# Kernel optimization log

Hardware: AMD Instinct MI355X
Metric: run time of the kernel (lower is better)

Reference implementation:

```python
import jax, jax.numpy as jnp
import numpy as np

B, T, C = 2, 4096, 768
H = 12
HD = C // H  # 64


def setup_inputs() -> dict:
    key = jax.random.key(0)
    k1, k2, k3 = jax.random.split(key, 3)
    scale = 0.02
    x = jax.random.normal(k1, (B, T, C), dtype=jnp.float32)
    w_attn = jax.random.normal(k2, (C, 3 * C), dtype=jnp.float32) * scale
    b_attn = jnp.zeros((3 * C,), dtype=jnp.float32)
    w_proj = jax.random.normal(k3, (C, C), dtype=jnp.float32) * scale
    b_proj = jnp.zeros((C,), dtype=jnp.float32)
    return {"x": x, "w_attn": w_attn, "b_attn": b_attn,
            "w_proj": w_proj, "b_proj": b_proj}


def reference(x, w_attn, b_attn, w_proj, b_proj):
    b, t, c = x.shape
    # QKV projection: (B,T,3C)
    qkv = x @ w_attn + b_attn
    q, k, v = jnp.split(qkv, 3, axis=2)
    # (B,H,T,HD)
    q = q.reshape(b, t, H, HD).transpose(0, 2, 1, 3)
    k = k.reshape(b, t, H, HD).transpose(0, 2, 1, 3)
    v = v.reshape(b, t, H, HD).transpose(0, 2, 1, 3)
    # scores: (B,H,T,T)
    scores = jnp.einsum('bhqd,bhkd->bhqk', q, k) / jnp.sqrt(jnp.float32(HD))
    causal = jnp.tril(jnp.ones((t, t), dtype=bool))
    scores = jnp.where(causal[None, None, :, :], scores, -jnp.inf)
    att = jax.nn.softmax(scores, axis=-1)
    # attn_dropout p=0 -> identity
    y = jnp.einsum('bhqk,bhkd->bhqd', att, v)
    y = y.transpose(0, 2, 1, 3).reshape(b, t, c)
    # output projection (resid_dropout p=0 -> identity)
    return y @ w_proj + b_proj
```

## Files before the change

kernel.cpp:

```cpp
#include <hip/hip_runtime.h>


typedef unsigned short u16;
typedef unsigned int u32;
using bf16x8 = __attribute__((ext_vector_type(8))) short;
using f32x4  = __attribute__((ext_vector_type(4))) float;

__device__ __forceinline__ float bf2f(u16 u) {
  return __uint_as_float(((u32)u) << 16);
}
__device__ __forceinline__ u16 f2bf(float f) {
  u32 u = __float_as_uint(f);
  u += 0x7fffu + ((u >> 16) & 1u);
  return (u16)(u >> 16);
}
__device__ __forceinline__ u32 cvtpk(float lo, float hi) {
  u32 r;
  asm("v_cvt_pk_bf16_f32 %0, %1, %2" : "=v"(r) : "v"(lo), "v"(hi));
  return r;
}
__device__ __forceinline__ void gload_lds16(const u16* g, u16* l) {
  __builtin_amdgcn_global_load_lds(
      (const __attribute__((address_space(1))) unsigned int*)g,
      (__attribute__((address_space(3))) unsigned int*)l, 16, 0, 0);
}

__global__ void fill_sentinel_f32(float* __restrict__ out, int n, float v) {
  const int i0 = blockIdx.x * blockDim.x + threadIdx.x;
  const int stride = gridDim.x * blockDim.x;
  for (int i = i0; i < n; i += stride) out[i] = v;
}

__global__ void convert_f32_bf16(const float* __restrict__ src, u16* __restrict__ dst,
                                 int n) {
  const int i0 = blockIdx.x * blockDim.x + threadIdx.x;
  const int stride = gridDim.x * blockDim.x;
  for (int i = i0; i < n; i += stride) dst[i] = f2bf(src[i]);
}

__global__ void transpose_f32_bf16(const float* __restrict__ in, u16* __restrict__ out,
                                   int R, int C) {
  __shared__ u16 tile[32][33];
  const int c0 = blockIdx.x * 32, r0 = blockIdx.y * 32;
  const int tx = threadIdx.x & 31, ty = threadIdx.x >> 5;
#pragma unroll
  for (int i = 0; i < 32; i += 8)
    tile[ty + i][tx] = f2bf(in[(size_t)(r0 + ty + i) * C + c0 + tx]);
  __syncthreads();
#pragma unroll
  for (int i = 0; i < 32; i += 8)
    out[(size_t)(c0 + ty + i) * R + r0 + tx] = tile[tx][ty + i];
}

#define QSCALE 0.18033688011112f

template <int MODE>
__global__ __launch_bounds__(256, 3)
void gemm128(const u16* __restrict__ A, const u16* __restrict__ Bt,
             const u16* __restrict__ bias, void* __restrict__ O0v,
             u16* __restrict__ O1, u16* __restrict__ O2, int Kd) {
  __shared__ __align__(16) u16 As[128 * 64];
  __shared__ __align__(16) u16 Bs[128 * 64];
  const int tid = threadIdx.x;
  const int lane = tid & 63, wave = tid >> 6;
  const int wm = wave >> 1, wn = wave & 1;
  const int l16 = lane & 15, quad = lane >> 4;

  const u16* Ag0 = A + (size_t)blockIdx.x * 128 * Kd +
                   (size_t)(tid >> 3) * Kd + (tid & 7) * 8;
  const u16* Bg0 = Bt + (size_t)blockIdx.y * 128 * Kd +
                   (size_t)(tid >> 3) * Kd + (tid & 7) * 8;
  const int ldsb = wave * 512;

  f32x4 acc[4][4] = {};
  for (int kt = 0; kt < Kd; kt += 64) {
#pragma unroll
    for (int i = 0; i < 4; ++i) {
      gload_lds16(Ag0 + (size_t)i * 32 * Kd + kt, &As[i * 2048 + ldsb]);
      gload_lds16(Bg0 + (size_t)i * 32 * Kd + kt, &Bs[i * 2048 + ldsb]);
    }
    __syncthreads();
#pragma unroll
    for (int s = 0; s < 2; ++s) {
      bf16x8 af[4], bfr[4];
#pragma unroll
      for (int i = 0; i < 4; ++i) {
        const int m = wm * 64 + i * 16 + l16;
        af[i] = *(const bf16x8*)&As[m * 64 + (s * 4 + quad) * 8];
        const int n = wn * 64 + i * 16 + l16;
        bfr[i] = *(const bf16x8*)&Bs[n * 64 + (s * 4 + quad) * 8];
      }
#pragma unroll
      for (int i = 0; i < 4; ++i)
#pragma unroll
        for (int j = 0; j < 4; ++j)
          acc[i][j] = __builtin_amdgcn_mfma_f32_16x16x32_bf16(af[i], bfr[j],
                                                              acc[i][j], 0, 0, 0);
    }
    __syncthreads();
  }

#pragma unroll
  for (int i = 0; i < 4; ++i) {
    const int mbase = blockIdx.x * 128 + wm * 64 + i * 16 + quad * 4;
#pragma unroll
    for (int j = 0; j < 4; ++j) {
      const int nb = blockIdx.y * 128 + wn * 64 + j * 16;
      const int n = nb + l16;
      const float bv = bf2f(bias[n]);
      if (MODE == 0) {
        const int which = nb / 768;
        const int b = mbase >> 12, t = mbase & 4095;
        const int c = n - which * 768;
        const int h = c >> 6, d = c & 63;
        const size_t bh = (size_t)b * 12 + h;
        if (which == 0) {
#pragma unroll
          for (int r = 0; r < 4; ++r)
            ((u16*)O0v)[((bh * 4096 + t + r) << 6) + d] =
                f2bf((acc[i][j][r] + bv) * QSCALE);
        } else if (which == 1) {
#pragma unroll
          for (int r = 0; r < 4; ++r)
            O1[((bh * 4096 + t + r) << 6) + d] = f2bf(acc[i][j][r] + bv);
        } else {
          ushort4 pk;
          pk.x = f2bf(acc[i][j][0] + bv);
          pk.y = f2bf(acc[i][j][1] + bv);
          pk.z = f2bf(acc[i][j][2] + bv);
          pk.w = f2bf(acc[i][j][3] + bv);
          *(ushort4*)&O2[((bh << 6) + (size_t)d) * 4096 + t] = pk;
        }
      } else {
#pragma unroll
        for (int r = 0; r < 4; ++r)
          ((float*)O0v)[(size_t)(mbase + r) * 768 + n] = acc[i][j][r] + bv;
      }
    }
  }
}

__global__ __launch_bounds__(256, 3)
void attn_chunk(const u16* __restrict__ Q, const u16* __restrict__ K,
                const u16* __restrict__ Vt, u16* __restrict__ Y,
                u16* __restrict__ part_o, float* __restrict__ part_l) {
  const int idx = blockIdx.x;
  const int bh = idx % 24;
  const int cid = 79 - (idx / 24);
  int qt = 0, base = 0, nc = 1;
  for (int q = 0; q < 32; ++q) {
    const int c = (q >> 3) + 1;
    if (cid < base + c) { qt = q; nc = c; break; }
    base += c;
  }
  const int j = cid - base;
  const int Nt = 2 * qt + 2;
  const int kbeg = j * 16;
  const int kend = (kbeg + 16 < Nt) ? kbeg + 16 : Nt;
  const int q0 = qt * 128;
  const int b = bh / 12, h = bh % 12;
  const size_t ho = (size_t)bh * 4096 * 64;
  const u16* Qg = Q + ho + (size_t)q0 * 64;
  const u16* Kg = K + ho;
  const u16* Vg = Vt + ho;

  __shared__ __align__(16) u16 Ks[3][64 * 64];
  __shared__ __align__(16) u16 Vs[3][64 * 64];

  const int tid = threadIdx.x;
  const int lane = tid & 63, wave = tid >> 6;
  const int l16 = lane & 15, quad = lane >> 4;
  const int sw8 = (l16 & 7) * 8;

  const int rl = tid >> 3, m7 = tid & 7;
  const int cs = (m7 ^ (rl & 7)) * 8;
  const u16* kg0 = Kg + (size_t)rl * 64 + cs;
  const u16* vg0 = Vg + (size_t)rl * 4096 + cs;
  const int wb = wave * 512;

  bf16x8 qf[2][2];
#pragma unroll
  for (int rt = 0; rt < 2; ++rt)
#pragma unroll
    for (int s = 0; s < 2; ++s)
      qf[rt][s] = *(const bf16x8*)&Qg[(wave * 32 + rt * 16 + l16) * 64 + s * 32 + quad * 8];

  bf16x8 ones;
#pragma unroll
  for (int e = 0; e < 8; ++e) ones[e] = (short)0x3F80;

  f32x4 lacc[2] = {};
  f32x4 o[2][4] = {};

  auto stage = [&](int bf, int kt2) {
    const size_t ko = (size_t)kt2 * 4096;
    const int to = kt2 * 64;
    gload_lds16(kg0 + ko,               &Ks[bf][wb]);
    gload_lds16(kg0 + ko + 2048,        &Ks[bf][2048 + wb]);
    gload_lds16(vg0 + to,               &Vs[bf][wb]);
    gload_lds16(vg0 + to + 32 * 4096,   &Vs[bf][2048 + wb]);
  };

  const int ntt = kend - kbeg;
  stage(0, kbeg);
  if (ntt > 1) {
    stage(1, kbeg + 1);
    asm volatile("s_waitcnt vmcnt(4)" ::: "memory");
  } else {
    asm volatile("s_waitcnt vmcnt(0)" ::: "memory");
  }
  __builtin_amdgcn_sched_barrier(0);
  __builtin_amdgcn_s_barrier();
  int cur = 0;

  for (int kt2 = kbeg; kt2 < kend; ++kt2) {
    const int t0 = kt2 * 64;
    const bool pf = (kt2 + 2 < kend);
    if (pf) {
      int nb = cur + 2; if (nb >= 3) nb -= 3;
      stage(nb, kt2 + 2);
    }
    __builtin_amdgcn_sched_barrier(0);

    f32x4 sc[4][2] = {};
#pragma unroll
    for (int s = 0; s < 2; ++s) {
      bf16x8 kf[4];
#pragma unroll
      for (int nt = 0; nt < 4; ++nt)
        kf[nt] = *(const bf16x8*)&Ks[cur][(nt * 16 + l16) * 64 +
                                          ((s * 32 + quad * 8) ^ sw8)];
      __builtin_amdgcn_s_setprio(1);
#pragma unroll
      for (int nt = 0; nt < 4; ++nt)
#pragma unroll
        for (int rt = 0; rt < 2; ++rt)
          sc[nt][rt] = __builtin_amdgcn_mfma_f32_16x16x32_bf16(kf[nt], qf[rt][s],
                                                               sc[nt][rt], 0, 0, 0);
      __builtin_amdgcn_s_setprio(0);
    }

    u32 pw[4][2][2];
#pragma unroll
    for (int rt = 0; rt < 2; ++rt) {
      const int rowb = q0 + wave * 32 + rt * 16;
      if (t0 + 63 <= rowb) {
#pragma unroll
        for (int nt = 0; nt < 4; ++nt) {
          f32x4 p;
#pragma unroll
          for (int r = 0; r < 4; ++r)
            p[r] = __builtin_amdgcn_exp2f(sc[nt][rt][r]);
          pw[nt][rt][0] = cvtpk(p[0], p[1]);
          pw[nt][rt][1] = cvtpk(p[2], p[3]);
        }
      } else {
        const int qrow = rowb + l16;
#pragma unroll
        for (int nt = 0; nt < 4; ++nt) {
          f32x4 p;
#pragma unroll
          for (int r = 0; r < 4; ++r) {
            float pv = __builtin_amdgcn_exp2f(sc[nt][rt][r]);
            if (t0 + nt * 16 + quad * 4 + r > qrow) pv = 0.f;
            p[r] = pv;
          }
          pw[nt][rt][0] = cvtpk(p[0], p[1]);
          pw[nt][rt][1] = cvtpk(p[2], p[3]);
        }
      }
    }

#pragma unroll
    for (int s2 = 0; s2 < 2; ++s2) {
      bf16x8 vf[4];
#pragma unroll
      for (int dt = 0; dt < 4; ++dt) {
        const int vbase = (dt * 16 + l16) * 64;
        const int a1 = vbase + ((s2 * 32 + quad * 4) ^ sw8);
        union { uint2 hv[2]; bf16x8 v; } uv;
        uv.hv[0] = *(const uint2*)&Vs[cur][a1];
        uv.hv[1] = *(const uint2*)&Vs[cur][a1 ^ 16];
        vf[dt] = uv.v;
      }
#pragma unroll
      for (int rt = 0; rt < 2; ++rt) {
        union { u32 w[4]; bf16x8 v; } up;
        up.w[0] = pw[2 * s2][rt][0];
        up.w[1] = pw[2 * s2][rt][1];
        up.w[2] = pw[2 * s2 + 1][rt][0];
        up.w[3] = pw[2 * s2 + 1][rt][1];
        __builtin_amdgcn_s_setprio(1);
#pragma unroll
        for (int dt = 0; dt < 4; ++dt)
          o[rt][dt] = __builtin_amdgcn_mfma_f32_16x16x32_bf16(up.v, vf[dt],
                                                              o[rt][dt], 0, 0, 0);
        lacc[rt] = __builtin_amdgcn_mfma_f32_16x16x32_bf16(up.v, ones,
                                                           lacc[rt], 0, 0, 0);
        __builtin_amdgcn_s_setprio(0);
      }
    }

    if (kt2 + 1 < kend) {
      if (pf) asm volatile("s_waitcnt vmcnt(4)" ::: "memory");
      else    asm volatile("s_waitcnt vmcnt(0)" ::: "memory");
      __builtin_amdgcn_sched_barrier(0);
      __builtin_amdgcn_s_barrier();
      if (++cur == 3) cur = 0;
    }
  }

  if (nc == 1) {
#pragma unroll
    for (int rt = 0; rt < 2; ++rt)
#pragma unroll
      for (int r = 0; r < 4; ++r) {
        const float inv = 1.f / lacc[rt][r];
        const int t = q0 + wave * 32 + rt * 16 + quad * 4 + r;
#pragma unroll
        for (int dt = 0; dt < 4; ++dt)
          Y[((size_t)b * 4096 + t) * 768 + h * 64 + dt * 16 + l16] =
              f2bf(o[rt][dt][r] * inv);
      }
  } else {
    const int pslot = bh * 72 + (cid - 8);
    u16* po = part_o + (size_t)pslot * 8192;
    float* pl = part_l + pslot * 128;
#pragma unroll
    for (int rt = 0; rt < 2; ++rt)
#pragma unroll
      for (int r = 0; r < 4; ++r) {
        const int row = wave * 32 + rt * 16 + quad * 4 + r;
#pragma unroll
        for (int dt = 0; dt < 4; ++dt)
          po[row * 64 + dt * 16 + l16] = f2bf(o[rt][dt][r]);
        if (l16 == 0) pl[row] = lacc[rt][r];
      }
  }
}

__global__ __launch_bounds__(256, 8)
void attn_combine(const u16* __restrict__ part_o, const float* __restrict__ part_l,
                  u16* __restrict__ Y) {
  const int bh = blockIdx.x, qt = 8 + blockIdx.y;
  const int g = qt >> 3, i = qt & 7;
  const int nc = g + 1;
  const int base = 4 * g * (g + 1) + i * (g + 1);
  const int slot0 = bh * 72 + base - 8;
  const int b = bh / 12, h = bh % 12;
  const int q0 = qt * 128;
  for (int e = threadIdx.x; e < 8192; e += 256) {
    const int row = e >> 6, d = e & 63;
    float Os = 0.f, ls = 0.f;
    for (int c = 0; c < nc; ++c) {
      Os += bf2f(part_o[(size_t)(slot0 + c) * 8192 + e]);
      ls += part_l[(slot0 + c) * 128 + row];
    }
    Y[((size_t)b * 4096 + q0 + row) * 768 + h * 64 + d] = f2bf(Os / ls);
  }
}

extern "C" void kernel_launch(void* const* d_in, const int* in_sizes, int n_in,
                              void* d_out, int out_size, void* d_ws, size_t ws_size,
                              hipStream_t stream) {
  (void)in_sizes; (void)n_in;
  const float* x      = (const float*)d_in[0];
  const float* w_attn = (const float*)d_in[1];
  const float* b_attn = (const float*)d_in[2];
  const float* w_proj = (const float*)d_in[3];
  const float* b_proj = (const float*)d_in[4];
  float* out = (float*)d_out;

  char* ws = (char*)d_ws;
  size_t off = 0;
  auto alloc = [&](size_t bytes) -> void* {
    void* p = ws + off;
    off += (bytes + 255) & ~(size_t)255;
    return p;
  };
  u16* xb  = (u16*)alloc((size_t)8192 * 768 * 2);
  u16* WtA = (u16*)alloc((size_t)2304 * 768 * 2);
  u16* WtP = (u16*)alloc((size_t)768 * 768 * 2);
  u16* ba  = (u16*)alloc(2304 * 2);
  u16* bp  = (u16*)alloc(768 * 2);
  u16* Q   = (u16*)alloc((size_t)6291456 * 2);
  u16* Kp  = (u16*)alloc((size_t)6291456 * 2);
  u16* Vt  = (u16*)alloc((size_t)6291456 * 2);
  u16* Y   = (u16*)alloc((size_t)6291456 * 2);
  u16* part_o  = (u16*)alloc((size_t)24 * 72 * 8192 * 2);
  float* part_l = (float*)alloc((size_t)24 * 72 * 128 * 4);

  if (ws_size < off) {
    fill_sentinel_f32<<<256, 256, 0, stream>>>(out, out_size,
                                               100.0f + (float)(ws_size >> 20));
    return;
  }

  convert_f32_bf16<<<2048, 256, 0, stream>>>(x, xb, 8192 * 768);
  convert_f32_bf16<<<16, 256, 0, stream>>>(b_attn, ba, 2304);
  convert_f32_bf16<<<8, 256, 0, stream>>>(b_proj, bp, 768);
  transpose_f32_bf16<<<dim3(72, 24), 256, 0, stream>>>(w_attn, WtA, 768, 2304);
  transpose_f32_bf16<<<dim3(24, 24), 256, 0, stream>>>(w_proj, WtP, 768, 768);

  gemm128<0><<<dim3(64, 18), 256, 0, stream>>>(xb, WtA, ba, Q, Kp, Vt, 768);
  attn_chunk<<<1920, 256, 0, stream>>>(Q, Kp, Vt, Y, part_o, part_l);
  attn_combine<<<dim3(24, 24), 256, 0, stream>>>(part_o, part_l, Y);
  gemm128<1><<<dim3(64, 6), 256, 0, stream>>>(Y, WtP, bp, out, nullptr, nullptr, 768);
}
```

Measured before the change: 273.1 us.

## Fuse prep kernels and load V directly from global into registers

Result: slower. 573.6 us (+110.0%).

```diff
diff --git a/kernel.cpp b/kernel.cpp
--- a/kernel.cpp
+++ b/kernel.cpp
@@ -31,25 +31,44 @@
   for (int i = i0; i < n; i += stride) out[i] = v;
 }
 
-__global__ void convert_f32_bf16(const float* __restrict__ src, u16* __restrict__ dst,
-                                 int n) {
-  const int i0 = blockIdx.x * blockDim.x + threadIdx.x;
-  const int stride = gridDim.x * blockDim.x;
-  for (int i = i0; i < n; i += stride) dst[i] = f2bf(src[i]);
-}
-
-__global__ void transpose_f32_bf16(const float* __restrict__ in, u16* __restrict__ out,
-                                   int R, int C) {
+__global__ __launch_bounds__(256)
+void prep(const float* __restrict__ x, const float* __restrict__ w_attn,
+          const float* __restrict__ b_attn, const float* __restrict__ w_proj,
+          const float* __restrict__ b_proj, u16* __restrict__ xb,
+          u16* __restrict__ WtA, u16* __restrict__ WtP,
+          u16* __restrict__ ba, u16* __restrict__ bp) {
   __shared__ u16 tile[32][33];
-  const int c0 = blockIdx.x * 32, r0 = blockIdx.y * 32;
-  const int tx = threadIdx.x & 31, ty = threadIdx.x >> 5;
-#pragma unroll
-  for (int i = 0; i < 32; i += 8)
-    tile[ty + i][tx] = f2bf(in[(size_t)(r0 + ty + i) * C + c0 + tx]);
-  __syncthreads();
-#pragma unroll
-  for (int i = 0; i < 32; i += 8)
-    out[(size_t)(c0 + ty + i) * R + r0 + tx] = tile[tx][ty + i];
+  const int bid = blockIdx.x, tid = threadIdx.x;
+  if (bid < 2304) {
+    const float* in; u16* out; int R, C, bx, by;
+    if (bid < 1728) { in = w_attn; out = WtA; R = 768; C = 2304;
+                      bx = bid % 72; by = bid / 72; }
+    else            { in = w_proj; out = WtP; R = 768; C = 768;
+                      bx = (bid - 1728) % 24; by = (bid - 1728) / 24; }
+    const int c0 = bx * 32, r0 = by * 32;
+    const int tx = tid & 31, ty = tid >> 5;
+#pragma unroll
+    for (int i = 0; i < 32; i += 8)
+      tile[ty + i][tx] = f2bf(in[(size_t)(r0 + ty + i) * C + c0 + tx]);
+    __syncthreads();
+#pragma unroll
+    for (int i = 0; i < 32; i += 8)
+      out[(size_t)(c0 + ty + i) * R + r0 + tx] = tile[tx][ty + i];
+  } else if (bid < 3328) {
+    const int n4 = 8192 * 768 / 4;
+    const int i0 = (bid - 2304) * 256 + tid, stride = 1024 * 256;
+    const float4* src = (const float4*)x;
+    ushort4* dst = (ushort4*)xb;
+    for (int i = i0; i < n4; i += stride) {
+      const float4 v = src[i];
+      ushort4 o;
+      o.x = f2bf(v.x); o.y = f2bf(v.y); o.z = f2bf(v.z); o.w = f2bf(v.w);
+      dst[i] = o;
+    }
+  } else {
+    for (int i = tid; i < 2304; i += 256) ba[i] = f2bf(b_attn[i]);
+    for (int i = tid; i < 768; i += 256) bp[i] = f2bf(b_proj[i]);
+  }
 }
 
 #define QSCALE 0.18033688011112f
@@ -140,7 +159,7 @@
   }
 }
 
-__global__ __launch_bounds__(256, 3)
+__global__ __launch_bounds__(256, 4)
 void attn_chunk(const u16* __restrict__ Q, const u16* __restrict__ K,
                 const u16* __restrict__ Vt, u16* __restrict__ Y,
                 u16* __restrict__ part_o, float* __restrict__ part_l) {
@@ -165,7 +184,6 @@
   const u16* Vg = Vt + ho;
 
   __shared__ __align__(16) u16 Ks[3][64 * 64];
-  __shared__ __align__(16) u16 Vs[3][64 * 64];
 
   const int tid = threadIdx.x;
   const int lane = tid & 63, wave = tid >> 6;
@@ -175,8 +193,9 @@
   const int rl = tid >> 3, m7 = tid & 7;
   const int cs = (m7 ^ (rl & 7)) * 8;
   const u16* kg0 = Kg + (size_t)rl * 64 + cs;
-  const u16* vg0 = Vg + (size_t)rl * 4096 + cs;
   const int wb = wave * 512;
+
+  const u16* vbl = Vg + (size_t)l16 * 4096 + quad * 4;
 
   bf16x8 qf[2][2];
 #pragma unroll
@@ -194,18 +213,15 @@
 
   auto stage = [&](int bf, int kt2) {
     const size_t ko = (size_t)kt2 * 4096;
-    const int to = kt2 * 64;
-    gload_lds16(kg0 + ko,               &Ks[bf][wb]);
-    gload_lds16(kg0 + ko + 2048,        &Ks[bf][2048 + wb]);
-    gload_lds16(vg0 + to,               &Vs[bf][wb]);
-    gload_lds16(vg0 + to + 32 * 4096,   &Vs[bf][2048 + wb]);
+    gload_lds16(kg0 + ko,        &Ks[bf][wb]);
+    gload_lds16(kg0 + ko + 2048, &Ks[bf][2048 + wb]);
   };
 
   const int ntt = kend - kbeg;
   stage(0, kbeg);
   if (ntt > 1) {
     stage(1, kbeg + 1);
-    asm volatile("s_waitcnt vmcnt(4)" ::: "memory");
+    asm volatile("s_waitcnt vmcnt(2)" ::: "memory");
   } else {
     asm volatile("s_waitcnt vmcnt(0)" ::: "memory");
   }
@@ -216,6 +232,17 @@
   for (int kt2 = kbeg; kt2 < kend; ++kt2) {
     const int t0 = kt2 * 64;
     const bool pf = (kt2 + 2 < kend);
+
+    uint2 vld[4][2][2];
+#pragma unroll
+    for (int dt = 0; dt < 4; ++dt) {
+      const u16* vp = vbl + (size_t)dt * 65536 + t0;
+#pragma unroll
+      for (int s2 = 0; s2 < 2; ++s2)
+#pragma unroll
+        for (int hh = 0; hh < 2; ++hh)
+          vld[dt][s2][hh] = *(const uint2*)(vp + s2 * 32 + hh * 16);
+    }
     if (pf) {
       int nb = cur + 2; if (nb >= 3) nb -= 3;
       stage(nb, kt2 + 2);
@@ -271,18 +298,11 @@
       }
     }
 
+    if (pf) asm volatile("s_waitcnt vmcnt(2)" ::: "memory");
+    else    asm volatile("s_waitcnt vmcnt(0)" ::: "memory");
+
 #pragma unroll
     for (int s2 = 0; s2 < 2; ++s2) {
-      bf16x8 vf[4];
-#pragma unroll
-      for (int dt = 0; dt < 4; ++dt) {
-        const int vbase = (dt * 16 + l16) * 64;
-        const int a1 = vbase + ((s2 * 32 + quad * 4) ^ sw8);
-        union { uint2 hv[2]; bf16x8 v; } uv;
-        uv.hv[0] = *(const uint2*)&Vs[cur][a1];
-        uv.hv[1] = *(const uint2*)&Vs[cur][a1 ^ 16];
-        vf[dt] = uv.v;
-      }
 #pragma unroll
       for (int rt = 0; rt < 2; ++rt) {
         union { u32 w[4]; bf16x8 v; } up;
@@ -292,9 +312,13 @@
         up.w[3] = pw[2 * s2 + 1][rt][1];
         __builtin_amdgcn_s_setprio(1);
 #pragma unroll
-        for (int dt = 0; dt < 4; ++dt)
-          o[rt][dt] = __builtin_amdgcn_mfma_f32_16x16x32_bf16(up.v, vf[dt],
+        for (int dt = 0; dt < 4; ++dt) {
+          union { uint2 hv[2]; bf16x8 v; } uv;
+          uv.hv[0] = vld[dt][s2][0];
+          uv.hv[1] = vld[dt][s2][1];
+          o[rt][dt] = __builtin_amdgcn_mfma_f32_16x16x32_bf16(up.v, uv.v,
                                                               o[rt][dt], 0, 0, 0);
+        }
         lacc[rt] = __builtin_amdgcn_mfma_f32_16x16x32_bf16(up.v, ones,
                                                            lacc[rt], 0, 0, 0);
         __builtin_amdgcn_s_setprio(0);
@@ -302,9 +326,6 @@
     }
 
     if (kt2 + 1 < kend) {
-      if (pf) asm volatile("s_waitcnt vmcnt(4)" ::: "memory");
-      else    asm volatile("s_waitcnt vmcnt(0)" ::: "memory");
-      __builtin_amdgcn_sched_barrier(0);
       __builtin_amdgcn_s_barrier();
       if (++cur == 3) cur = 0;
     }
@@ -396,12 +417,8 @@
     return;
   }
 
-  convert_f32_bf16<<<2048, 256, 0, stream>>>(x, xb, 8192 * 768);
-  convert_f32_bf16<<<16, 256, 0, stream>>>(b_attn, ba, 2304);
-  convert_f32_bf16<<<8, 256, 0, stream>>>(b_proj, bp, 768);
-  transpose_f32_bf16<<<dim3(72, 24), 256, 0, stream>>>(w_attn, WtA, 768, 2304);
-  transpose_f32_bf16<<<dim3(24, 24), 256, 0, stream>>>(w_proj, WtP, 768, 768);
-
+  prep<<<3329, 256, 0, stream>>>(x, w_attn, b_attn, w_proj, b_proj,
+                                 xb, WtA, WtP, ba, bp);
   gemm128<0><<<dim3(64, 18), 256, 0, stream>>>(xb, WtA, ba, Q, Kp, Vt, 768);
   attn_chunk<<<1920, 256, 0, stream>>>(Q, Kp, Vt, Y, part_o, part_l);
   attn_combine<<<dim3(24, 24), 256, 0, stream>>>(part_o, part_l, Y);
```
